# Kernel tuning notes

Measured on AMD Instinct MI355X. Metric: run time of the kernel, lower is better.

## Reference

```python
import jax, jax.numpy as jnp
import numpy as np

B, S, D, H = 2, 2048, 256, 8

def setup_inputs() -> dict:
    key = jax.random.key(0)
    ks = jax.random.split(key, 7)
    inputs = jax.random.normal(ks[0], (B, S, D), dtype=jnp.float32)
    timestamp = jnp.sort(jax.random.randint(ks[1], (B, S), 0, 100000, dtype=jnp.int32), axis=-1)
    wQ = jax.random.normal(ks[2], (H, D, D), dtype=jnp.float32) * 0.05
    wK = jax.random.normal(ks[3], (H, D, D), dtype=jnp.float32) * 0.05
    wV = jax.random.normal(ks[4], (H, D, D), dtype=jnp.float32) * 0.05
    wO = jax.random.normal(ks[5], (H * D, D), dtype=jnp.float32) * 0.05
    theta = jax.random.uniform(ks[6], (1, 1), dtype=jnp.float32)
    return {"inputs": inputs, "timestamp": timestamp, "wQ": wQ, "wK": wK,
            "wV": wV, "wO": wO, "theta": theta}

def reference(inputs, timestamp, wQ, wK, wV, wO, theta):
    b, s, d = inputs.shape
    # per-head projections (original loops over heads via TensorArray; vectorized here)
    Q = jnp.einsum('bsd,hde->bhse', inputs, wQ)
    K = jnp.einsum('bsd,hde->bhse', inputs, wK)
    V = jnp.einsum('bsd,hde->bhse', inputs, wV)
    exp_x = jnp.einsum('bhsd,bhtd->bhst', Q, K) / jnp.sqrt(jnp.float32(d))  # [B,H,S,S]
    x = jax.nn.softmax(exp_x, axis=-1)
    low_tri = jnp.tril(jnp.ones((s, s), dtype=jnp.float32))
    x = x * low_tri
    x = x / jnp.sum(x, axis=-1, keepdims=True)  # causal renormalized softmax

    # time-decay double-softmax branch. NOTE: the original module computes `a`
    # but returns x @ V, so `a`/`s_`/`d_` do not affect the output (dead code,
    # reproduced here for fidelity; XLA will DCE it).
    ts = timestamp.astype(jnp.float32)
    d_t = ts[:, None, :, None] - ts[:, None, None, :]  # diag(t) - t : [B,1,S,S]
    decay = (1.0 - jnp.cumsum(x, axis=-1)) * d_t * low_tri
    s_ = exp_x * jnp.exp(-(theta[0, 0] * theta[0, 0]) * decay)
    a = jax.nn.softmax(s_, axis=-1) * low_tri
    a = a / jnp.sum(a, axis=-1, keepdims=True)
    del a  # unused in original output

    ret = jnp.einsum('bhst,bhtd->bhsd', x, V)          # [B,H,S,D]
    out = ret.transpose(0, 2, 1, 3).reshape(b, s, -1)  # concat heads -> [B,S,H*D]
    return out @ wO
```

## Files before the change

kernel.cpp:

```cpp
#include <hip/hip_runtime.h>
#include <cstdint>
#include <cstddef>

#define S_LEN 2048
#define DIM   256
#define NH    8
#define NB    2
#define HDIM  (NH * DIM)

using bf16 = __bf16;
typedef __bf16 bf16x8 __attribute__((ext_vector_type(8)));
typedef __bf16 bf16x4 __attribute__((ext_vector_type(4)));
typedef float  f32x4  __attribute__((ext_vector_type(4)));

typedef const __attribute__((address_space(1))) unsigned int* as1_u32p;
typedef __attribute__((address_space(3))) unsigned int* as3_u32p;

__device__ __forceinline__ void cp16(const bf16* g, bf16* l) {
    __builtin_amdgcn_global_load_lds((as1_u32p)g, (as3_u32p)l, 16, 0, 0);
}


__global__ __launch_bounds__(256) void cast_x_kernel(const float* __restrict__ in,
                                                     bf16* __restrict__ out) {
    int i = (blockIdx.x * 256 + threadIdx.x) * 4;
    float4 v = *(const float4*)(in + i);
    bf16x4 o;
    o[0] = (bf16)v.x; o[1] = (bf16)v.y; o[2] = (bf16)v.z; o[3] = (bf16)v.w;
    *(bf16x4*)(out + i) = o;
}

__global__ __launch_bounds__(256) void transpose_w3_kernel(const float* __restrict__ wQ,
                                                           const float* __restrict__ wK,
                                                           const float* __restrict__ wV,
                                                           bf16* __restrict__ WQt,
                                                           bf16* __restrict__ WKt,
                                                           bf16* __restrict__ WVt) {
    __shared__ float tile[64][65];
    const int z   = blockIdx.z;
    const int mat = z >> 3;
    const int h   = z & 7;
    const float* in = (mat == 0 ? wQ : mat == 1 ? wK : wV) + (size_t)h * DIM * DIM;
    bf16* out       = (mat == 0 ? WQt : mat == 1 ? WKt : WVt) + (size_t)h * DIM * DIM;
    const int c0 = blockIdx.x * 64, r0 = blockIdx.y * 64;
    const int tr  = threadIdx.x >> 4;
    const int tc4 = (threadIdx.x & 15) * 4;
    #pragma unroll
    for (int p = 0; p < 4; ++p) {
        int row = p * 16 + tr;
        float4 v = *(const float4*)(in + (size_t)(r0 + row) * DIM + c0 + tc4);
        tile[row][tc4+0] = v.x; tile[row][tc4+1] = v.y;
        tile[row][tc4+2] = v.z; tile[row][tc4+3] = v.w;
    }
    __syncthreads();
    #pragma unroll
    for (int p = 0; p < 4; ++p) {
        int orow = p * 16 + tr;
        bf16x4 o;
        #pragma unroll
        for (int j = 0; j < 4; ++j) o[j] = (bf16)tile[tc4 + j][orow];
        *(bf16x4*)(out + (size_t)(c0 + orow) * DIM + r0 + tc4) = o;
    }
}

__global__ __launch_bounds__(256) void transpose_cast_kernel(const float* __restrict__ in,
                                                             bf16* __restrict__ out,
                                                             int R, int C) {
    __shared__ float tile[64][65];
    const int c0 = blockIdx.x * 64, r0 = blockIdx.y * 64;
    const int tr  = threadIdx.x >> 4;
    const int tc4 = (threadIdx.x & 15) * 4;
    #pragma unroll
    for (int p = 0; p < 4; ++p) {
        int row = p * 16 + tr;
        float4 v = *(const float4*)(in + (size_t)(r0 + row) * C + c0 + tc4);
        tile[row][tc4+0] = v.x; tile[row][tc4+1] = v.y;
        tile[row][tc4+2] = v.z; tile[row][tc4+3] = v.w;
    }
    __syncthreads();
    #pragma unroll
    for (int p = 0; p < 4; ++p) {
        int orow = p * 16 + tr;
        bf16x4 o;
        #pragma unroll
        for (int j = 0; j < 4; ++j) o[j] = (bf16)tile[tc4 + j][orow];
        *(bf16x4*)(out + (size_t)(c0 + orow) * R + r0 + tc4) = o;
    }
}

template<int EPI>
__device__ __forceinline__ void gemm_tile(const bf16* __restrict__ A, const bf16* __restrict__ BT,
                                          void* __restrict__ C, bf16* As, bf16* Bs,
                                          int tm, int tn, int K, int lda, int ldb, int ldc)
{
    const int tid  = threadIdx.x;
    const int lane = tid & 63;
    const int wave = tid >> 6;
    const int wm   = (wave >> 1) << 6;
    const int wn   = (wave & 1) << 6;
    const int l16  = lane & 15;
    const int quad = lane >> 4;

    const int m0 = tm << 7, n0 = tn << 7;

    const int srow = (lane >> 2);
    const int gch  = (lane & 3) ^ (srow & 3);

    f32x4 acc[4][4] = {};

    const int ksteps = K >> 5;

    #pragma unroll
    for (int j = 0; j < 2; ++j) {
        const int g = wave*2 + j;
        cp16(A  + (size_t)(m0 + g*16 + srow)*lda + (gch << 3), As + g*512);
        cp16(BT + (size_t)(n0 + g*16 + srow)*ldb + (gch << 3), Bs + g*512);
    }

    for (int ks = 0; ks < ksteps; ++ks) {
        const int pb = ks & 1;
        asm volatile("s_waitcnt vmcnt(0)" ::: "memory");
        __syncthreads();
        if (ks + 1 < ksteps) {
            const int k1 = (ks + 1) << 5;
            #pragma unroll
            for (int j = 0; j < 2; ++j) {
                const int g = wave*2 + j;
                cp16(A  + (size_t)(m0 + g*16 + srow)*lda + k1 + (gch << 3),
                     As + (pb ^ 1)*4096 + g*512);
                cp16(BT + (size_t)(n0 + g*16 + srow)*ldb + k1 + (gch << 3),
                     Bs + (pb ^ 1)*4096 + g*512);
            }
        }
        const bf16* Ab = As + pb*4096;
        const bf16* Bb = Bs + pb*4096;
        bf16x8 af[4], bfv[4];
        #pragma unroll
        for (int i = 0; i < 4; ++i) {
            const int row = wm + i*16 + l16;
            af[i]  = *(const bf16x8*)(Ab + row*32 + ((quad ^ (l16 & 3)) << 3));
        }
        #pragma unroll
        for (int i = 0; i < 4; ++i) {
            const int row = wn + i*16 + l16;
            bfv[i] = *(const bf16x8*)(Bb + row*32 + ((quad ^ (l16 & 3)) << 3));
        }
        #pragma unroll
        for (int i = 0; i < 4; ++i)
            #pragma unroll
            for (int j = 0; j < 4; ++j)
                acc[i][j] = __builtin_amdgcn_mfma_f32_16x16x32_bf16(af[i], bfv[j], acc[i][j], 0, 0, 0);
    }

    #pragma unroll
    for (int i = 0; i < 4; ++i)
        #pragma unroll
        for (int j = 0; j < 4; ++j)
            #pragma unroll
            for (int r = 0; r < 4; ++r) {
                int mg = m0 + wm + i*16 + quad*4 + r;
                int ng = n0 + wn + j*16 + l16;
                float v = acc[i][j][r];
                if (EPI == 0)      ((bf16*)C)[(size_t)mg * ldc + ng] = (bf16)v;
                else if (EPI == 1) ((float*)C)[(size_t)mg * ldc + ng] = v;
                else               atomicAdd(&((float*)C)[(size_t)mg * ldc + ng], v);
            }
}

__global__ __launch_bounds__(256) void proj_kernel(const bf16* __restrict__ Xb,
    const bf16* __restrict__ WQt, const bf16* __restrict__ WKt, const bf16* __restrict__ WVt,
    bf16* __restrict__ Qg, bf16* __restrict__ Kg, bf16* __restrict__ VTg)
{
    __shared__ __align__(16) bf16 smem[4 * 4096];
    const int by  = blockIdx.y;
    const int mat = by >> 4;
    const int b   = (by >> 3) & 1;
    const int h   = by & 7;
    const int bx  = blockIdx.x;
    const bf16*  Xbb = Xb + (size_t)b * S_LEN * DIM;
    const size_t bh  = (size_t)(b * NH + h);
    if (mat == 0) {
        gemm_tile<0>(Xbb, WQt + (size_t)h*DIM*DIM, Qg + bh*S_LEN*DIM, smem, smem + 8192,
                     bx & 15, bx >> 4, DIM, DIM, DIM, DIM);
    } else if (mat == 1) {
        gemm_tile<0>(Xbb, WKt + (size_t)h*DIM*DIM, Kg + bh*S_LEN*DIM, smem, smem + 8192,
                     bx & 15, bx >> 4, DIM, DIM, DIM, DIM);
    } else {
        gemm_tile<0>(WVt + (size_t)h*DIM*DIM, Xbb, VTg + bh*DIM*S_LEN, smem, smem + 8192,
                     bx & 1, bx >> 1, DIM, DIM, DIM, S_LEN);
    }
}

__global__ __launch_bounds__(256) void outproj_kernel(const bf16* __restrict__ Ret,
                                                      const bf16* __restrict__ WOt,
                                                      float* __restrict__ out)
{
    __shared__ __align__(16) bf16 smem[4 * 4096];
    int bx = blockIdx.x;
    int t  = bx & 63;
    int kq = bx >> 6;
    gemm_tile<2>(Ret + kq*512, WOt + kq*512, out, smem, smem + 8192,
                 t >> 1, t & 1, 512, HDIM, HDIM, DIM);
}

__global__ __launch_bounds__(256) void attn_kernel(const bf16* __restrict__ Qg,
                                                   const bf16* __restrict__ Kg,
                                                   const bf16* __restrict__ VTg,
                                                   bf16* __restrict__ Ret,
                                                   bf16* __restrict__ Opart,
                                                   float* __restrict__ Lpart)
{
    __shared__ __align__(16) bf16 KsB[2][32 * 256];
    __shared__ __align__(16) bf16 VTs[256 * 32];
    __shared__ __align__(16) bf16 Ps [4 * 16 * 40];

    const int tid  = threadIdx.x;
    const int lane = tid & 63;
    const int wave = tid >> 6;
    const int l16  = lane & 15;
    const int quad = lane >> 4;

    const int bx = blockIdx.x;
    const int R  = (bx < 256) ? bx : (bx < 512 ? 767 - bx : bx);
    const int bh = R & 15;
    const int r  = R >> 4;
    int qt, s; bool split;
    if (r < 40) {
        const int g = r / 5, j = r % 5;
        if (j == 0)      { qt = 15 - g;     split = false; s = 0; }
        else if (j <= 2) { qt = 31 - 2*g;   split = true;  s = j - 1; }
        else             { qt = 30 - 2*g;   split = true;  s = j - 3; }
    } else { qt = 47 - r; split = false; s = 0; }
    const int b = bh >> 3, h = bh & 7;

    int kstep0, kstep1;
    if (split) { kstep0 = s * (qt + 1); kstep1 = kstep0 + qt + 1; }
    else       { kstep0 = 0;           kstep1 = 2*qt + 2; }

    const bf16* Qbh  = Qg  + (size_t)(b*NH + h) * S_LEN * DIM;
    const bf16* Kbh  = Kg  + (size_t)(b*NH + h) * S_LEN * DIM;
    const bf16* VTbh = VTg + (size_t)(b*NH + h) * DIM * S_LEN;

    const int qbase = qt * 64 + wave * 16;

    bf16x8 qf[8];
    #pragma unroll
    for (int kc = 0; kc < 8; ++kc)
        qf[kc] = *(const bf16x8*)(Qbh + (size_t)(qbase + l16)*DIM + kc*32 + quad*8);

    f32x4 o[16] = {};
    float l_part[4] = {0.f, 0.f, 0.f, 0.f};

    {
        const int t0 = kstep0 << 5;
        #pragma unroll
        for (int j = 0; j < 4; ++j) {
            const int sN = (((wave << 2) + j) << 6) + lane;
            const int ts = sN >> 5, cs = sN & 31;
            cp16(Kbh + (size_t)(t0 + ts)*DIM + ((cs ^ ts) << 3),
                 &KsB[0][0] + (((wave << 2) + j) << 9));
        }
    }

    for (int step = kstep0; step < kstep1; ++step) {
        const int pb = (step - kstep0) & 1;
        asm volatile("s_waitcnt vmcnt(0)" ::: "memory");
        __syncthreads();

        const int t0 = step << 5;
        #pragma unroll
        for (int j = 0; j < 4; ++j) {
            const int sN = (((wave << 2) + j) << 6) + lane;
            const int es = sN >> 2, cs = sN & 3;
            cp16(VTbh + (size_t)es*S_LEN + t0 + ((cs ^ ((es >> 1) & 3)) << 3),
                 &VTs[0] + (((wave << 2) + j) << 9));
        }
        if (step + 1 < kstep1) {
            const int t1 = (step + 1) << 5;
            #pragma unroll
            for (int j = 0; j < 4; ++j) {
                const int sN = (((wave << 2) + j) << 6) + lane;
                const int ts = sN >> 5, cs = sN & 31;
                cp16(Kbh + (size_t)(t1 + ts)*DIM + ((cs ^ ts) << 3),
                     &KsB[pb ^ 1][0] + (((wave << 2) + j) << 9));
            }
        }

        const bf16* KsP = &KsB[pb][0];

        f32x4 sacc[2] = {};
        #pragma unroll
        for (int kc = 0; kc < 8; ++kc) {
            const int ch = (kc << 2) + quad;
            bf16x8 b0 = *(const bf16x8*)(KsP + (l16 << 8)        + ((ch ^ l16) << 3));
            bf16x8 b1 = *(const bf16x8*)(KsP + ((16 + l16) << 8) + ((ch ^ (16 + l16)) << 3));
            sacc[0] = __builtin_amdgcn_mfma_f32_16x16x32_bf16(qf[kc], b0, sacc[0], 0,0,0);
            sacc[1] = __builtin_amdgcn_mfma_f32_16x16x32_bf16(qf[kc], b1, sacc[1], 0,0,0);
        }

        float pv[2][4];
        #pragma unroll
        for (int r2 = 0; r2 < 4; ++r2) {
            const int qgi = qbase + quad*4 + r2;
            const bool ok0 = (t0 + l16)      <= qgi;
            const bool ok1 = (t0 + 16 + l16) <= qgi;
            float p0 = ok0 ? __expf(sacc[0][r2] * 0.0625f) : 0.0f;
            float p1 = ok1 ? __expf(sacc[1][r2] * 0.0625f) : 0.0f;
            l_part[r2] += p0 + p1;
            pv[0][r2] = p0; pv[1][r2] = p1;
        }

        #pragma unroll
        for (int nt = 0; nt < 2; ++nt)
            #pragma unroll
            for (int r2 = 0; r2 < 4; ++r2)
                Ps[wave*640 + (quad*4 + r2)*40 + nt*16 + l16] = (bf16)pv[nt][r2];
        __syncthreads();

        bf16x8 pf = *(const bf16x8*)(Ps + wave*640 + l16*40 + quad*8);
        #pragma unroll
        for (int ct = 0; ct < 16; ++ct) {
            const int e = (ct << 4) + l16;
            bf16x8 vf = *(const bf16x8*)(&VTs[0] + (e << 5) + ((quad ^ ((e >> 1) & 3)) << 3));
            o[ct] = __builtin_amdgcn_mfma_f32_16x16x32_bf16(pf, vf, o[ct], 0,0,0);
        }
    }

    float lsum[4];
    #pragma unroll
    for (int r2 = 0; r2 < 4; ++r2) {
        float l = l_part[r2];
        l += __shfl_xor(l, 1);
        l += __shfl_xor(l, 2);
        l += __shfl_xor(l, 4);
        l += __shfl_xor(l, 8);
        lsum[r2] = l;
    }

    if (!split) {
        #pragma unroll
        for (int r2 = 0; r2 < 4; ++r2) {
            const int qgi = qbase + quad*4 + r2;
            const float inv = 1.0f / lsum[r2];
            #pragma unroll
            for (int ct = 0; ct < 16; ++ct)
                Ret[((size_t)b*S_LEN + qgi)*HDIM + h*DIM + ct*16 + l16] = (bf16)(o[ct][r2] * inv);
        }
    } else {
        const size_t slot = ((size_t)(bh*16 + (qt - 16)))*2 + s;
        bf16*  Ob = Opart + slot * (64*256);
        float* Lb = Lpart + slot * 64;
        #pragma unroll
        for (int r2 = 0; r2 < 4; ++r2) {
            const int trow = wave*16 + quad*4 + r2;
            #pragma unroll
            for (int ct = 0; ct < 16; ++ct)
                Ob[(size_t)trow*256 + ct*16 + l16] = (bf16)o[ct][r2];
            if (l16 == 0) Lb[trow] = lsum[r2];
        }
    }
}

__global__ __launch_bounds__(256) void combine_kernel(const bf16* __restrict__ Opart,
                                                      const float* __restrict__ Lpart,
                                                      bf16* __restrict__ Ret)
{
    const int bx  = blockIdx.x;
    const int bh  = bx >> 4;
    const int qti = bx & 15;
    const int b = bh >> 3, h = bh & 7;
    const int row  = threadIdx.x >> 2;
    const int col0 = (threadIdx.x & 3) * 64;

    const size_t slot0 = ((size_t)(bh*16 + qti))*2;
    const bf16* O0 = Opart + slot0 * (64*256) + (size_t)row*256 + col0;
    const bf16* O1 = O0 + 64*256;
    const float inv = 1.0f / (Lpart[slot0*64 + row] + Lpart[(slot0+1)*64 + row]);

    const int q = (qti + 16)*64 + row;
    bf16* dst = Ret + ((size_t)b*S_LEN + q)*HDIM + h*DIM + col0;
    #pragma unroll
    for (int ch = 0; ch < 8; ++ch) {
        bf16x8 a = *(const bf16x8*)(O0 + ch*8);
        bf16x8 c = *(const bf16x8*)(O1 + ch*8);
        bf16x8 w;
        #pragma unroll
        for (int j = 0; j < 8; ++j) w[j] = (bf16)(((float)a[j] + (float)c[j]) * inv);
        *(bf16x8*)(dst + ch*8) = w;
    }
}


extern "C" void kernel_launch(void* const* d_in, const int* in_sizes, int n_in,
                              void* d_out, int out_size, void* d_ws, size_t ws_size,
                              hipStream_t stream)
{
    (void)in_sizes; (void)n_in; (void)ws_size;
    const float* X  = (const float*)d_in[0];
    const float* wQ = (const float*)d_in[2];
    const float* wK = (const float*)d_in[3];
    const float* wV = (const float*)d_in[4];
    const float* wO = (const float*)d_in[5];

    char* ws = (char*)d_ws;
    const size_t MB = 1u << 20;
    bf16*  Xb    = (bf16*)(ws + 0*MB);
    bf16*  WQt   = (bf16*)(ws + 2*MB);
    bf16*  WKt   = (bf16*)(ws + 3*MB);
    bf16*  WVt   = (bf16*)(ws + 4*MB);
    bf16*  WOt   = (bf16*)(ws + 5*MB);
    bf16*  Qg    = (bf16*)(ws + 6*MB);
    bf16*  Kg    = (bf16*)(ws + 22*MB);
    bf16*  VTg   = (bf16*)(ws + 38*MB);
    bf16*  Ret   = (bf16*)(ws + 54*MB);
    bf16*  Opart = (bf16*)(ws + 70*MB);
    float* Lpart = (float*)(ws + 86*MB);

    hipMemsetAsync(d_out, 0, (size_t)out_size * sizeof(float), stream);

    cast_x_kernel        <<<1024, 256, 0, stream>>>(X, Xb);
    transpose_w3_kernel  <<<dim3(4, 4, 24), 256, 0, stream>>>(wQ, wK, wV, WQt, WKt, WVt);
    transpose_cast_kernel<<<dim3(4, 32),    256, 0, stream>>>(wO, WOt, HDIM, DIM);
    proj_kernel    <<<dim3(32, 48), 256, 0, stream>>>(Xb, WQt, WKt, WVt, Qg, Kg, VTg);
    attn_kernel    <<<768,          256, 0, stream>>>(Qg, Kg, VTg, Ret, Opart, Lpart);
    combine_kernel <<<256,          256, 0, stream>>>(Opart, Lpart, Ret);
    outproj_kernel <<<256,          256, 0, stream>>>(Ret, WOt, (float*)d_out);
}
```

Baseline: 192.8 us.

## Use two waves of 32 query rows each in attention for K/V fragment reuse

```diff
diff --git a/kernel.cpp b/kernel.cpp
--- a/kernel.cpp
+++ b/kernel.cpp
@@ -203,16 +203,16 @@
                  t >> 1, t & 1, 512, HDIM, HDIM, DIM);
 }
 
-__global__ __launch_bounds__(256) void attn_kernel(const bf16* __restrict__ Qg,
-                                                   const bf16* __restrict__ Kg,
-                                                   const bf16* __restrict__ VTg,
-                                                   bf16* __restrict__ Ret,
-                                                   bf16* __restrict__ Opart,
-                                                   float* __restrict__ Lpart)
+__global__ __launch_bounds__(128, 2) void attn_kernel(const bf16* __restrict__ Qg,
+                                                      const bf16* __restrict__ Kg,
+                                                      const bf16* __restrict__ VTg,
+                                                      bf16* __restrict__ Ret,
+                                                      bf16* __restrict__ Opart,
+                                                      float* __restrict__ Lpart)
 {
     __shared__ __align__(16) bf16 KsB[2][32 * 256];
     __shared__ __align__(16) bf16 VTs[256 * 32];
-    __shared__ __align__(16) bf16 Ps [4 * 16 * 40];
+    __shared__ __align__(16) bf16 Ps [2 * 32 * 40];
 
     const int tid  = threadIdx.x;
     const int lane = tid & 63;
@@ -241,24 +241,26 @@
     const bf16* Kbh  = Kg  + (size_t)(b*NH + h) * S_LEN * DIM;
     const bf16* VTbh = VTg + (size_t)(b*NH + h) * DIM * S_LEN;
 
-    const int qbase = qt * 64 + wave * 16;
-
-    bf16x8 qf[8];
-    #pragma unroll
-    for (int kc = 0; kc < 8; ++kc)
-        qf[kc] = *(const bf16x8*)(Qbh + (size_t)(qbase + l16)*DIM + kc*32 + quad*8);
-
-    f32x4 o[16] = {};
-    float l_part[4] = {0.f, 0.f, 0.f, 0.f};
+    const int qbase = qt * 64 + wave * 32;
+
+    bf16x8 qf[2][8];
+    #pragma unroll
+    for (int rs = 0; rs < 2; ++rs)
+        #pragma unroll
+        for (int kc = 0; kc < 8; ++kc)
+            qf[rs][kc] = *(const bf16x8*)(Qbh + (size_t)(qbase + rs*16 + l16)*DIM + kc*32 + quad*8);
+
+    f32x4 o[2][16] = {};
+    float l_part[2][4] = {};
 
     {
-        const int t0 = kstep0 << 5;
-        #pragma unroll
-        for (int j = 0; j < 4; ++j) {
-            const int sN = (((wave << 2) + j) << 6) + lane;
+        const int t00 = kstep0 << 5;
+        #pragma unroll
+        for (int j = 0; j < 8; ++j) {
+            const int sN = (((wave << 3) + j) << 6) + lane;
             const int ts = sN >> 5, cs = sN & 31;
-            cp16(Kbh + (size_t)(t0 + ts)*DIM + ((cs ^ ts) << 3),
-                 &KsB[0][0] + (((wave << 2) + j) << 9));
+            cp16(Kbh + (size_t)(t00 + ts)*DIM + ((cs ^ ts) << 3),
+                 &KsB[0][0] + (((wave << 3) + j) << 9));
         }
     }
 
@@ -269,95 +271,100 @@
 
         const int t0 = step << 5;
         #pragma unroll
-        for (int j = 0; j < 4; ++j) {
-            const int sN = (((wave << 2) + j) << 6) + lane;
+        for (int j = 0; j < 8; ++j) {
+            const int sN = (((wave << 3) + j) << 6) + lane;
             const int es = sN >> 2, cs = sN & 3;
             cp16(VTbh + (size_t)es*S_LEN + t0 + ((cs ^ ((es >> 1) & 3)) << 3),
-                 &VTs[0] + (((wave << 2) + j) << 9));
+                 &VTs[0] + (((wave << 3) + j) << 9));
         }
         if (step + 1 < kstep1) {
             const int t1 = (step + 1) << 5;
             #pragma unroll
-            for (int j = 0; j < 4; ++j) {
-                const int sN = (((wave << 2) + j) << 6) + lane;
+            for (int j = 0; j < 8; ++j) {
+                const int sN = (((wave << 3) + j) << 6) + lane;
                 const int ts = sN >> 5, cs = sN & 31;
                 cp16(Kbh + (size_t)(t1 + ts)*DIM + ((cs ^ ts) << 3),
-                     &KsB[pb ^ 1][0] + (((wave << 2) + j) << 9));
+                     &KsB[pb ^ 1][0] + (((wave << 3) + j) << 9));
             }
         }
 
         const bf16* KsP = &KsB[pb][0];
 
-        f32x4 sacc[2] = {};
+        f32x4 sacc[2][2] = {};
         #pragma unroll
         for (int kc = 0; kc < 8; ++kc) {
             const int ch = (kc << 2) + quad;
             bf16x8 b0 = *(const bf16x8*)(KsP + (l16 << 8)        + ((ch ^ l16) << 3));
             bf16x8 b1 = *(const bf16x8*)(KsP + ((16 + l16) << 8) + ((ch ^ (16 + l16)) << 3));
-            sacc[0] = __builtin_amdgcn_mfma_f32_16x16x32_bf16(qf[kc], b0, sacc[0], 0,0,0);
-            sacc[1] = __builtin_amdgcn_mfma_f32_16x16x32_bf16(qf[kc], b1, sacc[1], 0,0,0);
-        }
-
-        float pv[2][4];
-        #pragma unroll
-        for (int r2 = 0; r2 < 4; ++r2) {
-            const int qgi = qbase + quad*4 + r2;
-            const bool ok0 = (t0 + l16)      <= qgi;
-            const bool ok1 = (t0 + 16 + l16) <= qgi;
-            float p0 = ok0 ? __expf(sacc[0][r2] * 0.0625f) : 0.0f;
-            float p1 = ok1 ? __expf(sacc[1][r2] * 0.0625f) : 0.0f;
-            l_part[r2] += p0 + p1;
-            pv[0][r2] = p0; pv[1][r2] = p1;
-        }
-
-        #pragma unroll
-        for (int nt = 0; nt < 2; ++nt)
-            #pragma unroll
-            for (int r2 = 0; r2 < 4; ++r2)
-                Ps[wave*640 + (quad*4 + r2)*40 + nt*16 + l16] = (bf16)pv[nt][r2];
+            sacc[0][0] = __builtin_amdgcn_mfma_f32_16x16x32_bf16(qf[0][kc], b0, sacc[0][0], 0,0,0);
+            sacc[0][1] = __builtin_amdgcn_mfma_f32_16x16x32_bf16(qf[1][kc], b0, sacc[0][1], 0,0,0);
+            sacc[1][0] = __builtin_amdgcn_mfma_f32_16x16x32_bf16(qf[0][kc], b1, sacc[1][0], 0,0,0);
+            sacc[1][1] = __builtin_amdgcn_mfma_f32_16x16x32_bf16(qf[1][kc], b1, sacc[1][1], 0,0,0);
+        }
+
+        #pragma unroll
+        for (int rs = 0; rs < 2; ++rs)
+            #pragma unroll
+            for (int kt = 0; kt < 2; ++kt)
+                #pragma unroll
+                for (int r2 = 0; r2 < 4; ++r2) {
+                    const int qgi = qbase + rs*16 + quad*4 + r2;
+                    const bool ok = (t0 + kt*16 + l16) <= qgi;
+                    float p = ok ? __expf(sacc[kt][rs][r2] * 0.0625f) : 0.0f;
+                    l_part[rs][r2] += p;
+                    Ps[wave*1280 + (rs*16 + quad*4 + r2)*40 + kt*16 + l16] = (bf16)p;
+                }
         __syncthreads();
 
-        bf16x8 pf = *(const bf16x8*)(Ps + wave*640 + l16*40 + quad*8);
+        bf16x8 pf0 = *(const bf16x8*)(Ps + wave*1280 + l16*40 + quad*8);
+        bf16x8 pf1 = *(const bf16x8*)(Ps + wave*1280 + (16 + l16)*40 + quad*8);
         #pragma unroll
         for (int ct = 0; ct < 16; ++ct) {
             const int e = (ct << 4) + l16;
             bf16x8 vf = *(const bf16x8*)(&VTs[0] + (e << 5) + ((quad ^ ((e >> 1) & 3)) << 3));
-            o[ct] = __builtin_amdgcn_mfma_f32_16x16x32_bf16(pf, vf, o[ct], 0,0,0);
-        }
-    }
-
-    float lsum[4];
-    #pragma unroll
-    for (int r2 = 0; r2 < 4; ++r2) {
-        float l = l_part[r2];
-        l += __shfl_xor(l, 1);
-        l += __shfl_xor(l, 2);
-        l += __shfl_xor(l, 4);
-        l += __shfl_xor(l, 8);
-        lsum[r2] = l;
-    }
+            o[0][ct] = __builtin_amdgcn_mfma_f32_16x16x32_bf16(pf0, vf, o[0][ct], 0,0,0);
+            o[1][ct] = __builtin_amdgcn_mfma_f32_16x16x32_bf16(pf1, vf, o[1][ct], 0,0,0);
+        }
+    }
+
+    float lsum[2][4];
+    #pragma unroll
+    for (int rs = 0; rs < 2; ++rs)
+        #pragma unroll
+        for (int r2 = 0; r2 < 4; ++r2) {
+            float l = l_part[rs][r2];
+            l += __shfl_xor(l, 1);
+            l += __shfl_xor(l, 2);
+            l += __shfl_xor(l, 4);
+            l += __shfl_xor(l, 8);
+            lsum[rs][r2] = l;
+        }
 
     if (!split) {
         #pragma unroll
-        for (int r2 = 0; r2 < 4; ++r2) {
-            const int qgi = qbase + quad*4 + r2;
-            const float inv = 1.0f / lsum[r2];
-            #pragma unroll
-            for (int ct = 0; ct < 16; ++ct)
-                Ret[((size_t)b*S_LEN + qgi)*HDIM + h*DIM + ct*16 + l16] = (bf16)(o[ct][r2] * inv);
-        }
+        for (int rs = 0; rs < 2; ++rs)
+            #pragma unroll
+            for (int r2 = 0; r2 < 4; ++r2) {
+                const int qgi = qbase + rs*16 + quad*4 + r2;
+                const float inv = 1.0f / lsum[rs][r2];
+                #pragma unroll
+                for (int ct = 0; ct < 16; ++ct)
+                    Ret[((size_t)b*S_LEN + qgi)*HDIM + h*DIM + ct*16 + l16] = (bf16)(o[rs][ct][r2] * inv);
+            }
     } else {
         const size_t slot = ((size_t)(bh*16 + (qt - 16)))*2 + s;
         bf16*  Ob = Opart + slot * (64*256);
         float* Lb = Lpart + slot * 64;
         #pragma unroll
-        for (int r2 = 0; r2 < 4; ++r2) {
-            const int trow = wave*16 + quad*4 + r2;
-            #pragma unroll
-            for (int ct = 0; ct < 16; ++ct)
-                Ob[(size_t)trow*256 + ct*16 + l16] = (bf16)o[ct][r2];
-            if (l16 == 0) Lb[trow] = lsum[r2];
-        }
+        for (int rs = 0; rs < 2; ++rs)
+            #pragma unroll
+            for (int r2 = 0; r2 < 4; ++r2) {
+                const int trow = wave*32 + rs*16 + quad*4 + r2;
+                #pragma unroll
+                for (int ct = 0; ct < 16; ++ct)
+                    Ob[(size_t)trow*256 + ct*16 + l16] = (bf16)o[rs][ct][r2];
+                if (l16 == 0) Lb[trow] = lsum[rs][r2];
+            }
     }
 }
 
@@ -422,7 +429,7 @@
     transpose_w3_kernel  <<<dim3(4, 4, 24), 256, 0, stream>>>(wQ, wK, wV, WQt, WKt, WVt);
     transpose_cast_kernel<<<dim3(4, 32),    256, 0, stream>>>(wO, WOt, HDIM, DIM);
     proj_kernel    <<<dim3(32, 48), 256, 0, stream>>>(Xb, WQt, WKt, WVt, Qg, Kg, VTg);
-    attn_kernel    <<<768,          256, 0, stream>>>(Qg, Kg, VTg, Ret, Opart, Lpart);
+    attn_kernel    <<<768,          128, 0, stream>>>(Qg, Kg, VTg, Ret, Opart, Lpart);
     combine_kernel <<<256,          256, 0, stream>>>(Opart, Lpart, Ret);
     outproj_kernel <<<256,          256, 0, stream>>>(Ret, WOt, (float*)d_out);
 }
```

Result: slower. 419.5 us (+117.6%).

## Repartition PV matmul so each wave owns a column slice across all rows

Applied to the files above, without the earlier changes.

```diff
diff --git a/kernel.cpp b/kernel.cpp
--- a/kernel.cpp
+++ b/kernel.cpp
@@ -242,22 +242,23 @@
     const bf16* VTbh = VTg + (size_t)(b*NH + h) * DIM * S_LEN;
 
     const int qbase = qt * 64 + wave * 16;
+    const int colw  = wave << 6;
 
     bf16x8 qf[8];
     #pragma unroll
     for (int kc = 0; kc < 8; ++kc)
         qf[kc] = *(const bf16x8*)(Qbh + (size_t)(qbase + l16)*DIM + kc*32 + quad*8);
 
-    f32x4 o[16] = {};
+    f32x4 o[4][4] = {};
     float l_part[4] = {0.f, 0.f, 0.f, 0.f};
 
     {
-        const int t0 = kstep0 << 5;
+        const int t00 = kstep0 << 5;
         #pragma unroll
         for (int j = 0; j < 4; ++j) {
             const int sN = (((wave << 2) + j) << 6) + lane;
             const int ts = sN >> 5, cs = sN & 31;
-            cp16(Kbh + (size_t)(t0 + ts)*DIM + ((cs ^ ts) << 3),
+            cp16(Kbh + (size_t)(t00 + ts)*DIM + ((cs ^ ts) << 3),
                  &KsB[0][0] + (((wave << 2) + j) << 9));
         }
     }
@@ -317,13 +318,20 @@
                 Ps[wave*640 + (quad*4 + r2)*40 + nt*16 + l16] = (bf16)pv[nt][r2];
         __syncthreads();
 
-        bf16x8 pf = *(const bf16x8*)(Ps + wave*640 + l16*40 + quad*8);
-        #pragma unroll
-        for (int ct = 0; ct < 16; ++ct) {
-            const int e = (ct << 4) + l16;
-            bf16x8 vf = *(const bf16x8*)(&VTs[0] + (e << 5) + ((quad ^ ((e >> 1) & 3)) << 3));
-            o[ct] = __builtin_amdgcn_mfma_f32_16x16x32_bf16(pf, vf, o[ct], 0,0,0);
-        }
+        bf16x8 pf[4], vf[4];
+        #pragma unroll
+        for (int rt = 0; rt < 4; ++rt)
+            pf[rt] = *(const bf16x8*)(Ps + rt*640 + l16*40 + quad*8);
+        #pragma unroll
+        for (int c2 = 0; c2 < 4; ++c2) {
+            const int e = colw + (c2 << 4) + l16;
+            vf[c2] = *(const bf16x8*)(&VTs[0] + (e << 5) + ((quad ^ ((e >> 1) & 3)) << 3));
+        }
+        #pragma unroll
+        for (int rt = 0; rt < 4; ++rt)
+            #pragma unroll
+            for (int c2 = 0; c2 < 4; ++c2)
+                o[rt][c2] = __builtin_amdgcn_mfma_f32_16x16x32_bf16(pf[rt], vf[c2], o[rt][c2], 0,0,0);
     }
 
     float lsum[4];
@@ -337,27 +345,43 @@
         lsum[r2] = l;
     }
 
+    __syncthreads();
+    float* Lsh = (float*)Ps;
+    if (l16 == 0) {
+        #pragma unroll
+        for (int r2 = 0; r2 < 4; ++r2) Lsh[wave*16 + quad*4 + r2] = lsum[r2];
+    }
+    __syncthreads();
+
     if (!split) {
         #pragma unroll
-        for (int r2 = 0; r2 < 4; ++r2) {
-            const int qgi = qbase + quad*4 + r2;
-            const float inv = 1.0f / lsum[r2];
-            #pragma unroll
-            for (int ct = 0; ct < 16; ++ct)
-                Ret[((size_t)b*S_LEN + qgi)*HDIM + h*DIM + ct*16 + l16] = (bf16)(o[ct][r2] * inv);
-        }
+        for (int rt = 0; rt < 4; ++rt)
+            #pragma unroll
+            for (int r2 = 0; r2 < 4; ++r2) {
+                const int row = rt*16 + quad*4 + r2;
+                const float inv = 1.0f / Lsh[row];
+                #pragma unroll
+                for (int c2 = 0; c2 < 4; ++c2)
+                    Ret[((size_t)b*S_LEN + qt*64 + row)*HDIM + h*DIM + colw + c2*16 + l16]
+                        = (bf16)(o[rt][c2][r2] * inv);
+            }
     } else {
         const size_t slot = ((size_t)(bh*16 + (qt - 16)))*2 + s;
         bf16*  Ob = Opart + slot * (64*256);
         float* Lb = Lpart + slot * 64;
-        #pragma unroll
-        for (int r2 = 0; r2 < 4; ++r2) {
-            const int trow = wave*16 + quad*4 + r2;
-            #pragma unroll
-            for (int ct = 0; ct < 16; ++ct)
-                Ob[(size_t)trow*256 + ct*16 + l16] = (bf16)o[ct][r2];
-            if (l16 == 0) Lb[trow] = lsum[r2];
-        }
+        if (l16 == 0) {
+            #pragma unroll
+            for (int r2 = 0; r2 < 4; ++r2) Lb[wave*16 + quad*4 + r2] = lsum[r2];
+        }
+        #pragma unroll
+        for (int rt = 0; rt < 4; ++rt)
+            #pragma unroll
+            for (int r2 = 0; r2 < 4; ++r2) {
+                const int row = rt*16 + quad*4 + r2;
+                #pragma unroll
+                for (int c2 = 0; c2 < 4; ++c2)
+                    Ob[(size_t)row*256 + colw + c2*16 + l16] = (bf16)o[rt][c2][r2];
+            }
     }
 }
 
```

Result: no change. 192.3 us (-0.3%).
